# Optimization experiments

Hardware: AMD Instinct MI355X
Metric: run time of the kernel (lower is better)

The kernel has to match this reference:

```python
import jax, jax.numpy as jnp
import numpy as np

D_MODEL = 1024
NUM_HEADS = 16
THETA = 10000.0


def _rope(x, pos):
    # x: [B, H, S, d_k], pos: [B, S] int
    d = x.shape[-1]
    half = d // 2
    inv_freq = THETA ** (-(jnp.arange(half, dtype=jnp.float32) * 2.0) / d)  # [half]
    ang = pos.astype(jnp.float32)[..., None] * inv_freq                     # [B, S, half]
    cos = jnp.cos(ang)[:, None, :, :]  # [B, 1, S, half]
    sin = jnp.sin(ang)[:, None, :, :]
    x1 = x[..., 0::2]
    x2 = x[..., 1::2]
    r1 = x1 * cos - x2 * sin
    r2 = x1 * sin + x2 * cos
    return jnp.stack([r1, r2], axis=-1).reshape(x.shape)


def setup_inputs() -> dict:
    key = jax.random.key(0)
    ks = jax.random.split(key, 5)
    B, S, D = 2, 2048, D_MODEL
    scale = 1.0 / np.sqrt(D)
    x = jax.random.normal(ks[0], (B, S, D), dtype=jnp.float32)
    token_positions = jnp.broadcast_to(jnp.arange(S, dtype=jnp.int32), (B, S))
    Wq = jax.random.normal(ks[1], (D, D), dtype=jnp.float32) * scale
    Wk = jax.random.normal(ks[2], (D, D), dtype=jnp.float32) * scale
    Wv = jax.random.normal(ks[3], (D, D), dtype=jnp.float32) * scale
    Wo = jax.random.normal(ks[4], (D, D), dtype=jnp.float32) * scale
    return {"x": x, "token_positions": token_positions, "Wq": Wq, "Wk": Wk, "Wv": Wv, "Wo": Wo}


def reference(x, token_positions, Wq, Wk, Wv, Wo):
    B, S, D = x.shape
    H = NUM_HEADS
    dk = D // H
    # Linear: y = x @ W.T (torch nn.Linear convention, no bias)
    q = jnp.einsum('bsd,od->bso', x, Wq).reshape(B, S, H, dk).transpose(0, 2, 1, 3)
    k = jnp.einsum('bsd,od->bso', x, Wk).reshape(B, S, H, dk).transpose(0, 2, 1, 3)
    v = jnp.einsum('bsd,od->bso', x, Wv).reshape(B, S, H, dk).transpose(0, 2, 1, 3)
    q = _rope(q, token_positions)
    k = _rope(k, token_positions)
    scores = jnp.einsum('bhqd,bhkd->bhqk', q, k) / jnp.sqrt(jnp.float32(dk))
    causal = jnp.tril(jnp.ones((S, S), dtype=bool))
    scores = jnp.where(causal, scores, jnp.finfo(scores.dtype).min)
    attn = jax.nn.softmax(scores, axis=-1)
    out = jnp.einsum('bhqk,bhkd->bhqd', attn, v)  # [B, H, S, dk]
    out = out.transpose(0, 2, 1, 3).reshape(B, S, D)
    return jnp.einsum('bsd,od->bso', out, Wo)
```

## Files before the change

kernel.cpp:

```cpp
#include <hip/hip_runtime.h>
#include <stdint.h>

#define S_LEN 2048
#define DMODEL 1024
#define NHEAD 16
#define DK 64
#define BATCH 2

typedef __attribute__((ext_vector_type(8))) short bf16x8;
typedef __attribute__((ext_vector_type(4))) float f32x4;

__device__ __forceinline__ unsigned short f2bf(float f) {
  union { float f; unsigned u; } x; x.f = f;
  unsigned u = x.u;
  return (unsigned short)((u + 0x7fffu + ((u >> 16) & 1u)) >> 16);
}

__device__ __forceinline__ uint cvt_pk_bf16(float a, float b) {
  uint r;
  asm("v_cvt_pk_bf16_f32 %0, %1, %2" : "=v"(r) : "v"(a), "v"(b));
  return r;
}

__device__ __forceinline__ void gload_lds16(const void* g, void* l) {
  __builtin_amdgcn_global_load_lds(
      (const __attribute__((address_space(1))) unsigned int*)g,
      (__attribute__((address_space(3))) unsigned int*)l, 16, 0, 0);
}

#define QSCALE 0.18033688011112042f

__global__ __launch_bounds__(256) void cast_inputs(
    const float4* __restrict__ x,
    const float4* __restrict__ wq, const float4* __restrict__ wk,
    const float4* __restrict__ wv, const float4* __restrict__ wo,
    ushort4* __restrict__ xb, ushort4* __restrict__ wqkvb, ushort4* __restrict__ wob,
    const int* __restrict__ pos, float2* __restrict__ rope)
{
  int i = blockIdx.x * 256 + threadIdx.x;
  const int NCAST = (1 << 21);
  if (i < NCAST) {
    float4 v; ushort4* dst;
    if (i < (1 << 20)) {
      v = x[i]; dst = xb + i;
    } else {
      int j = i - (1 << 20);
      int wsel = j >> 18;
      int o = j & ((1 << 18) - 1);
      const float4* src = (wsel == 0) ? wq : (wsel == 1) ? wk : (wsel == 2) ? wv : wo;
      v = src[o];
      dst = (wsel < 3) ? (wqkvb + ((size_t)wsel << 18) + o) : (wob + o);
    }
    ushort4 r;
    r.x = f2bf(v.x); r.y = f2bf(v.y); r.z = f2bf(v.z); r.w = f2bf(v.w);
    *dst = r;
  } else {
    int idx = i - NCAST;
    if (idx < 4096 * 32) {
      int ps = idx >> 5;
      int fi = idx & 31;
      float p = (float)pos[ps];
      float freq = exp2f(-(float)fi * 0.41524101186092096f);
      float ang = p * freq;
      rope[idx] = make_float2(cosf(ang), sinf(ang));
    }
  }
}

__global__ __launch_bounds__(256) void gemm_qkv(
    const ushort* __restrict__ A, const ushort* __restrict__ Bw,
    const float2* __restrict__ rope,
    ushort* __restrict__ Qb, ushort* __restrict__ Kb, ushort* __restrict__ Vg)
{
  constexpr int Kdim = 1024;
  __shared__ ushort At[128 * 64];
  __shared__ ushort Bt[128 * 64];
  const int bm = blockIdx.x & 31;
  const int bn = blockIdx.x >> 5;
  const int tid = threadIdx.x;
  const int w = tid >> 6, lane = tid & 63;
  const int wr = w >> 1, wc = w & 1;
  const int lrow = lane >> 3;
  const int lch = lane & 7;

  f32x4 acc[4][4];
#pragma unroll
  for (int i = 0; i < 4; ++i)
#pragma unroll
    for (int j = 0; j < 4; ++j) acc[i][j] = (f32x4){0.f, 0.f, 0.f, 0.f};

  const size_t abase = (size_t)(bm * 128) * Kdim;
  const size_t bbase = (size_t)(bn * 128) * Kdim;

  for (int kt = 0; kt < Kdim / 64; ++kt) {
#pragma unroll
    for (int inst = 0; inst < 4; ++inst) {
      int r = w * 32 + inst * 8 + lrow;
      int gc = lch ^ (r & 7);
      gload_lds16(A + abase + (size_t)r * Kdim + kt * 64 + gc * 8,
                  &At[(w * 32 + inst * 8) * 64]);
      gload_lds16(Bw + bbase + (size_t)r * Kdim + kt * 64 + gc * 8,
                  &Bt[(w * 32 + inst * 8) * 64]);
    }
    __syncthreads();
    __builtin_amdgcn_s_setprio(1);
#pragma unroll
    for (int kk = 0; kk < 2; ++kk) {
      bf16x8 af[4], bfv[4];
      int ch = kk * 4 + (lane >> 4);
#pragma unroll
      for (int fm = 0; fm < 4; ++fm) {
        int row = wr * 64 + fm * 16 + (lane & 15);
        af[fm] = *(const bf16x8*)&At[row * 64 + ((ch ^ (row & 7)) << 3)];
      }
#pragma unroll
      for (int fn = 0; fn < 4; ++fn) {
        int row = wc * 64 + fn * 16 + (lane & 15);
        bfv[fn] = *(const bf16x8*)&Bt[row * 64 + ((ch ^ (row & 7)) << 3)];
      }
#pragma unroll
      for (int fm = 0; fm < 4; ++fm)
#pragma unroll
        for (int fn = 0; fn < 4; ++fn)
          acc[fm][fn] = __builtin_amdgcn_mfma_f32_16x16x32_bf16(
              af[fm], bfv[fn], acc[fm][fn], 0, 0, 0);
    }
    __builtin_amdgcn_s_setprio(0);
    __syncthreads();
  }

  const int sel = bn >> 3;
  if (sel == 2) {
#pragma unroll
    for (int fn = 0; fn < 4; ++fn) {
      int gn = bn * 128 + wc * 64 + fn * 16 + (lane & 15);
      int col = gn & 1023;
      int h = col >> 6, d = col & 63;
#pragma unroll
      for (int fm = 0; fm < 4; ++fm) {
        int gm0 = bm * 128 + wr * 64 + fm * 16 + ((lane >> 4) << 2);
        int b = gm0 >> 11, s0 = gm0 & 2047;
        uint lo = cvt_pk_bf16(acc[fm][fn][0], acc[fm][fn][1]);
        uint hi2 = cvt_pk_bf16(acc[fm][fn][2], acc[fm][fn][3]);
        uint2 val; val.x = lo; val.y = hi2;
        *(uint2*)(Vg + ((size_t)((b * NHEAD + h) * DK + d) * S_LEN) + s0) = val;
      }
    }
  } else {
    ushort* dst0 = (sel == 0) ? Qb : Kb;
#pragma unroll
    for (int fn = 0; fn < 4; ++fn) {
      int gn = bn * 128 + wc * 64 + fn * 16 + (lane & 15);
      int col = gn & 1023;
      int h = col >> 6, d = col & 63;
#pragma unroll
      for (int fm = 0; fm < 4; ++fm) {
        int gm0 = bm * 128 + wr * 64 + fm * 16 + ((lane >> 4) << 2);
#pragma unroll
        for (int j = 0; j < 4; ++j) {
          int gm = gm0 + j;
          float v = acc[fm][fn][j];
          float p = __shfl_xor(v, 1);
          float2 cs = rope[gm * 32 + (d >> 1)];
          float r = (d & 1) ? (v * cs.x + p * cs.y) : (v * cs.x - p * cs.y);
          if (sel == 0) r *= QSCALE;
          int b = gm >> 11, s = gm & 2047;
          dst0[((size_t)(b * NHEAD + h) * S_LEN + s) * DK + d] = f2bf(r);
        }
      }
    }
  }
}

__global__ __launch_bounds__(256) void gemm_out64(
    const ushort* __restrict__ A, const ushort* __restrict__ Bw,
    float* __restrict__ Out)
{
  constexpr int Kdim = 1024;
  __shared__ ushort At[64 * 64];
  __shared__ ushort Bt[128 * 64];
  const int bm = blockIdx.x & 63;
  const int bn = blockIdx.x >> 6;
  const int tid = threadIdx.x;
  const int w = tid >> 6, lane = tid & 63;
  const int wr = w >> 1, wc = w & 1;
  const int lrow = lane >> 3;
  const int lch = lane & 7;

  f32x4 acc[2][4];
#pragma unroll
  for (int i = 0; i < 2; ++i)
#pragma unroll
    for (int j = 0; j < 4; ++j) acc[i][j] = (f32x4){0.f, 0.f, 0.f, 0.f};

  const size_t abase = (size_t)(bm * 64) * Kdim;
  const size_t bbase = (size_t)(bn * 128) * Kdim;

  for (int kt = 0; kt < Kdim / 64; ++kt) {
#pragma unroll
    for (int inst = 0; inst < 2; ++inst) {
      int r = inst * 32 + w * 8 + lrow;
      int gc = lch ^ (r & 7);
      gload_lds16(A + abase + (size_t)r * Kdim + kt * 64 + gc * 8,
                  &At[(inst * 32 + w * 8) * 64]);
    }
#pragma unroll
    for (int inst = 0; inst < 4; ++inst) {
      int r = inst * 32 + w * 8 + lrow;
      int gc = lch ^ (r & 7);
      gload_lds16(Bw + bbase + (size_t)r * Kdim + kt * 64 + gc * 8,
                  &Bt[(inst * 32 + w * 8) * 64]);
    }
    __syncthreads();
    __builtin_amdgcn_s_setprio(1);
#pragma unroll
    for (int kk = 0; kk < 2; ++kk) {
      bf16x8 af[2], bfv[4];
      int ch = kk * 4 + (lane >> 4);
#pragma unroll
      for (int fm = 0; fm < 2; ++fm) {
        int row = wr * 32 + fm * 16 + (lane & 15);
        af[fm] = *(const bf16x8*)&At[row * 64 + ((ch ^ (row & 7)) << 3)];
      }
#pragma unroll
      for (int fn = 0; fn < 4; ++fn) {
        int row = wc * 64 + fn * 16 + (lane & 15);
        bfv[fn] = *(const bf16x8*)&Bt[row * 64 + ((ch ^ (row & 7)) << 3)];
      }
#pragma unroll
      for (int fm = 0; fm < 2; ++fm)
#pragma unroll
        for (int fn = 0; fn < 4; ++fn)
          acc[fm][fn] = __builtin_amdgcn_mfma_f32_16x16x32_bf16(
              af[fm], bfv[fn], acc[fm][fn], 0, 0, 0);
    }
    __builtin_amdgcn_s_setprio(0);
    __syncthreads();
  }

#pragma unroll
  for (int fn = 0; fn < 4; ++fn) {
    int gn = bn * 128 + wc * 64 + fn * 16 + (lane & 15);
#pragma unroll
    for (int fm = 0; fm < 2; ++fm) {
      int gm0 = bm * 64 + wr * 32 + fm * 16 + ((lane >> 4) << 2);
#pragma unroll
      for (int j = 0; j < 4; ++j)
        Out[(size_t)(gm0 + j) * 1024 + gn] = acc[fm][fn][j];
    }
  }
}

__global__ __launch_bounds__(256) void attn_kernel(
    const ushort* __restrict__ Qb, const ushort* __restrict__ Kb,
    const ushort* __restrict__ Vg, ushort* __restrict__ Ob)
{
  __shared__ ushort Kt[2][64 * 64];
  __shared__ ushort Vt[2][64 * 64];
  __shared__ ushort Pt[4][16 * 64];
  const int tid = threadIdx.x;
  const int w = tid >> 6, lane = tid & 63;
  const int g = lane >> 4, q = lane & 15;
  const int ww = w & 1;
  const int bid = blockIdx.x;
  const int swz = (bid & 7) * 128 + (bid >> 3);
  const int bh = swz >> 5;
  const int pair = (swz >> 1) & 15;
  const int half = swz & 1;
  const size_t kqbase = (size_t)bh * (S_LEN * DK);
  const size_t vbase  = (size_t)bh * (DK * S_LEN);
  const int b = bh >> 4, h = bh & 15;
  const int qtw = (w < 2) ? (31 - pair) : pair;
  const int ktmax = 31 - pair;
  const int qrow0 = qtw * 64 + half * 32 + ww * 16;
  ushort* Pw = Pt[w];
  uint* Pw32 = (uint*)Pw;

  bf16x8 qf[2];
  {
    const ushort* qp = Qb + kqbase + (size_t)(qrow0 + q) * DK + g * 8;
    qf[0] = *(const bf16x8*)qp;
    qf[1] = *(const bf16x8*)(qp + 32);
  }
  f32x4 oacc[4];
#pragma unroll
  for (int dt = 0; dt < 4; ++dt) oacc[dt] = (f32x4){0.f, 0.f, 0.f, 0.f};
  float m_r = -INFINITY, l_r = 0.f;

#define STAGE(buf_, kt_)                                                     \
  do {                                                                       \
    _Pragma("unroll") for (int pass = 0; pass < 2; ++pass) {                 \
      int r0 = pass * 32 + w * 8;                                            \
      int r = r0 + (lane >> 3);                                              \
      int gc = (lane & 7) ^ (r & 7);                                         \
      gload_lds16(Kb + kqbase + (size_t)((kt_) * 64 + r) * DK + gc * 8,      \
                  &Kt[buf_][r0 * 64]);                                       \
      gload_lds16(Vg + vbase + (size_t)r * S_LEN + (kt_) * 64 + gc * 8,      \
                  &Vt[buf_][r0 * 64]);                                       \
    }                                                                        \
  } while (0)

  STAGE(0, 0);
  __syncthreads();

  int cur = 0;
  for (int kt = 0; kt <= ktmax; ++kt) {
    if (kt < ktmax) STAGE(cur ^ 1, kt + 1);

    if (kt <= qtw) {
      f32x4 sacc[4];
#pragma unroll
      for (int ct = 0; ct < 4; ++ct) sacc[ct] = (f32x4){0.f, 0.f, 0.f, 0.f};
      __builtin_amdgcn_s_setprio(1);
#pragma unroll
      for (int kk = 0; kk < 2; ++kk) {
        int ch = kk * 4 + g;
#pragma unroll
        for (int ct = 0; ct < 4; ++ct) {
          int row = ct * 16 + q;
          bf16x8 kf = *(const bf16x8*)&Kt[cur][row * 64 + ((ch ^ (row & 7)) << 3)];
          sacc[ct] = __builtin_amdgcn_mfma_f32_16x16x32_bf16(kf, qf[kk], sacc[ct], 0, 0, 0);
        }
      }
      __builtin_amdgcn_s_setprio(0);

      if (kt == qtw) {
        int qa = qrow0 + q;
#pragma unroll
        for (int ct = 0; ct < 4; ++ct) {
#pragma unroll
          for (int j = 0; j < 4; ++j) {
            int kv = qtw * 64 + ct * 16 + g * 4 + j;
            if (kv > qa) sacc[ct][j] = -INFINITY;
          }
        }
      }

      float mx = sacc[0][0];
#pragma unroll
      for (int ct = 0; ct < 4; ++ct)
#pragma unroll
        for (int j = 0; j < 4; ++j) mx = fmaxf(mx, sacc[ct][j]);
      mx = fmaxf(mx, __shfl_xor(mx, 16));
      mx = fmaxf(mx, __shfl_xor(mx, 32));
      if (mx > m_r + 8.0f) {
        float sc = exp2f(m_r - mx);
        m_r = mx;
        l_r *= sc;
#pragma unroll
        for (int dt = 0; dt < 4; ++dt)
#pragma unroll
          for (int j = 0; j < 4; ++j) oacc[dt][j] *= sc;
      }
      float p[4][4];
      float rs = 0.f;
#pragma unroll
      for (int ct = 0; ct < 4; ++ct)
#pragma unroll
        for (int j = 0; j < 4; ++j) {
          float e = exp2f(sacc[ct][j] - m_r);
          p[ct][j] = e; rs += e;
        }
      rs += __shfl_xor(rs, 16);
      rs += __shfl_xor(rs, 32);
      l_r += rs;

#pragma unroll
      for (int ct = 0; ct < 4; ++ct)
#pragma unroll
        for (int i = 0; i < 2; ++i) {
          uint u = cvt_pk_bf16(p[ct][2 * i], p[ct][2 * i + 1]);
          int idx = 8 * ct + 2 * g + i;
          Pw32[q * 32 + (((idx >> 2) ^ (q & 7)) << 2) + (idx & 3)] = u;
        }
      __builtin_amdgcn_s_setprio(1);
#pragma unroll
      for (int kk = 0; kk < 2; ++kk) {
        int ch = kk * 4 + g;
        bf16x8 pb = *(const bf16x8*)&Pw[q * 64 + ((ch ^ (q & 7)) << 3)];
#pragma unroll
        for (int dt = 0; dt < 4; ++dt) {
          int vr = dt * 16 + q;
          bf16x8 vf = *(const bf16x8*)&Vt[cur][vr * 64 + ((ch ^ (vr & 7)) << 3)];
          oacc[dt] = __builtin_amdgcn_mfma_f32_16x16x32_bf16(vf, pb, oacc[dt], 0, 0, 0);
        }
      }
      __builtin_amdgcn_s_setprio(0);
    }

    __syncthreads();
    cur ^= 1;
  }

  float inv = 1.0f / l_r;
#pragma unroll
  for (int dt = 0; dt < 4; ++dt)
#pragma unroll
    for (int i = 0; i < 2; ++i) {
      uint u = cvt_pk_bf16(oacc[dt][2 * i] * inv, oacc[dt][2 * i + 1] * inv);
      int idx = dt * 8 + 2 * g + i;
      Pw32[q * 32 + (((idx >> 2) ^ (q & 7)) << 2) + (idx & 3)] = u;
    }
#pragma unroll
  for (int pass = 0; pass < 2; ++pass) {
    int qr = pass * 8 + (lane >> 3), c = lane & 7;
    bf16x8 vv = *(const bf16x8*)&Pw[qr * 64 + ((c ^ (qr & 7)) << 3)];
    *(bf16x8*)(Ob + ((size_t)(b * S_LEN) + qrow0 + qr) * DMODEL + h * DK + c * 8) = vv;
  }
#undef STAGE
}

extern "C" void kernel_launch(void* const* d_in, const int* in_sizes, int n_in,
                              void* d_out, int out_size, void* d_ws, size_t ws_size,
                              hipStream_t stream) {
  const float* x  = (const float*)d_in[0];
  const int* pos  = (const int*)d_in[1];
  const float* wq = (const float*)d_in[2];
  const float* wk = (const float*)d_in[3];
  const float* wv = (const float*)d_in[4];
  const float* wo = (const float*)d_in[5];
  float* out = (float*)d_out;

  char* ws = (char*)d_ws;
  ushort* xb    = (ushort*)(ws);
  ushort* wqkvb = (ushort*)(ws + (size_t)( 8u << 20));
  ushort* wob   = (ushort*)(ws + (size_t)(14u << 20));
  float2* rope  = (float2*)(ws + (size_t)(16u << 20));
  ushort* Qb    = (ushort*)(ws + (size_t)(17u << 20));
  ushort* Kb    = (ushort*)(ws + (size_t)(25u << 20));
  ushort* Vg    = (ushort*)(ws + (size_t)(33u << 20));
  ushort* Ob    = (ushort*)(ws + (size_t)(41u << 20));

  cast_inputs<<<8704, 256, 0, stream>>>((const float4*)x, (const float4*)wq,
      (const float4*)wk, (const float4*)wv, (const float4*)wo,
      (ushort4*)xb, (ushort4*)wqkvb, (ushort4*)wob, pos, rope);
  gemm_qkv<<<32 * 24, 256, 0, stream>>>(xb, wqkvb, rope, Qb, Kb, Vg);
  attn_kernel<<<1024, 256, 0, stream>>>(Qb, Kb, Vg, Ob);
  gemm_out64<<<512, 256, 0, stream>>>(Ob, wob, out);
}
```

Measured before the change: 127.3 us.

## Process paired query tiles sequentially per block with full 64-row tiles

Each attention block now handles two complementary query tiles (pair and 31-pair) one after the other, with all four waves covering 64 query rows, instead of splitting waves across two tiles in a shared KV loop. This halves the grid and lets every staged K/V tile be used by all four waves, removing the idle waves that skipped causal tiles. The row-sum cross-lane shuffle is also moved out of the inner loop to a single reduction at the end. The cost is fewer blocks and two serialized KV sweeps per block.

```diff
diff --git a/kernel.cpp b/kernel.cpp
--- a/kernel.cpp
+++ b/kernel.cpp
@@ -261,53 +261,56 @@
   const int tid = threadIdx.x;
   const int w = tid >> 6, lane = tid & 63;
   const int g = lane >> 4, q = lane & 15;
-  const int ww = w & 1;
   const int bid = blockIdx.x;
-  const int swz = (bid & 7) * 128 + (bid >> 3);
-  const int bh = swz >> 5;
-  const int pair = (swz >> 1) & 15;
-  const int half = swz & 1;
+  const int swz = (bid & 7) * 64 + (bid >> 3);
+  const int bh = swz >> 4, pair = swz & 15;
   const size_t kqbase = (size_t)bh * (S_LEN * DK);
   const size_t vbase  = (size_t)bh * (DK * S_LEN);
   const int b = bh >> 4, h = bh & 15;
-  const int qtw = (w < 2) ? (31 - pair) : pair;
-  const int ktmax = 31 - pair;
-  const int qrow0 = qtw * 64 + half * 32 + ww * 16;
   ushort* Pw = Pt[w];
   uint* Pw32 = (uint*)Pw;
 
-  bf16x8 qf[2];
-  {
-    const ushort* qp = Qb + kqbase + (size_t)(qrow0 + q) * DK + g * 8;
-    qf[0] = *(const bf16x8*)qp;
-    qf[1] = *(const bf16x8*)(qp + 32);
-  }
-  f32x4 oacc[4];
-#pragma unroll
-  for (int dt = 0; dt < 4; ++dt) oacc[dt] = (f32x4){0.f, 0.f, 0.f, 0.f};
-  float m_r = -INFINITY, l_r = 0.f;
-
-#define STAGE(buf_, kt_)                                                     \
-  do {                                                                       \
-    _Pragma("unroll") for (int pass = 0; pass < 2; ++pass) {                 \
-      int r0 = pass * 32 + w * 8;                                            \
-      int r = r0 + (lane >> 3);                                              \
-      int gc = (lane & 7) ^ (r & 7);                                         \
-      gload_lds16(Kb + kqbase + (size_t)((kt_) * 64 + r) * DK + gc * 8,      \
-                  &Kt[buf_][r0 * 64]);                                       \
-      gload_lds16(Vg + vbase + (size_t)r * S_LEN + (kt_) * 64 + gc * 8,      \
-                  &Vt[buf_][r0 * 64]);                                       \
-    }                                                                        \
-  } while (0)
-
-  STAGE(0, 0);
-  __syncthreads();
-
-  int cur = 0;
-  for (int kt = 0; kt <= ktmax; ++kt) {
-    if (kt < ktmax) STAGE(cur ^ 1, kt + 1);
-
-    if (kt <= qtw) {
+  for (int t2 = 0; t2 < 2; ++t2) {
+    const int qt = t2 ? (31 - pair) : pair;
+    const int qrow0 = qt * 64 + w * 16;
+
+    bf16x8 qf[2];
+    {
+      const ushort* qp = Qb + kqbase + (size_t)(qrow0 + q) * DK + g * 8;
+      qf[0] = *(const bf16x8*)qp;
+      qf[1] = *(const bf16x8*)(qp + 32);
+    }
+    f32x4 oacc[4];
+#pragma unroll
+    for (int dt = 0; dt < 4; ++dt) oacc[dt] = (f32x4){0.f, 0.f, 0.f, 0.f};
+    float m_r = -INFINITY, l_r = 0.f;
+
+#pragma unroll
+    for (int pass = 0; pass < 2; ++pass) {
+      int r0 = pass * 32 + w * 8;
+      int r = r0 + (lane >> 3);
+      int gc = (lane & 7) ^ (r & 7);
+      gload_lds16(Kb + kqbase + (size_t)r * DK + gc * 8, &Kt[0][r0 * 64]);
+      gload_lds16(Vg + vbase + (size_t)r * S_LEN + gc * 8, &Vt[0][r0 * 64]);
+    }
+    __syncthreads();
+
+    int cur = 0;
+    for (int kt = 0; kt <= qt; ++kt) {
+      if (kt < qt) {
+        int nxt = cur ^ 1, ktn = kt + 1;
+#pragma unroll
+        for (int pass = 0; pass < 2; ++pass) {
+          int r0 = pass * 32 + w * 8;
+          int r = r0 + (lane >> 3);
+          int gc = (lane & 7) ^ (r & 7);
+          gload_lds16(Kb + kqbase + (size_t)(ktn * 64 + r) * DK + gc * 8,
+                      &Kt[nxt][r0 * 64]);
+          gload_lds16(Vg + vbase + (size_t)r * S_LEN + ktn * 64 + gc * 8,
+                      &Vt[nxt][r0 * 64]);
+        }
+      }
+
       f32x4 sacc[4];
 #pragma unroll
       for (int ct = 0; ct < 4; ++ct) sacc[ct] = (f32x4){0.f, 0.f, 0.f, 0.f};
@@ -324,13 +327,13 @@
       }
       __builtin_amdgcn_s_setprio(0);
 
-      if (kt == qtw) {
+      if (kt == qt) {
         int qa = qrow0 + q;
 #pragma unroll
         for (int ct = 0; ct < 4; ++ct) {
 #pragma unroll
           for (int j = 0; j < 4; ++j) {
-            int kv = qtw * 64 + ct * 16 + g * 4 + j;
+            int kv = qt * 64 + ct * 16 + g * 4 + j;
             if (kv > qa) sacc[ct][j] = -INFINITY;
           }
         }
@@ -361,8 +364,6 @@
           float e = exp2f(sacc[ct][j] - m_r);
           p[ct][j] = e; rs += e;
         }
-      rs += __shfl_xor(rs, 16);
-      rs += __shfl_xor(rs, 32);
       l_r += rs;
 
 #pragma unroll
@@ -386,28 +387,29 @@
         }
       }
       __builtin_amdgcn_s_setprio(0);
-    }
-
-    __syncthreads();
-    cur ^= 1;
-  }
-
-  float inv = 1.0f / l_r;
-#pragma unroll
-  for (int dt = 0; dt < 4; ++dt)
-#pragma unroll
-    for (int i = 0; i < 2; ++i) {
-      uint u = cvt_pk_bf16(oacc[dt][2 * i] * inv, oacc[dt][2 * i + 1] * inv);
-      int idx = dt * 8 + 2 * g + i;
-      Pw32[q * 32 + (((idx >> 2) ^ (q & 7)) << 2) + (idx & 3)] = u;
-    }
-#pragma unroll
-  for (int pass = 0; pass < 2; ++pass) {
-    int qr = pass * 8 + (lane >> 3), c = lane & 7;
-    bf16x8 vv = *(const bf16x8*)&Pw[qr * 64 + ((c ^ (qr & 7)) << 3)];
-    *(bf16x8*)(Ob + ((size_t)(b * S_LEN) + qrow0 + qr) * DMODEL + h * DK + c * 8) = vv;
-  }
-#undef STAGE
+      __syncthreads();
+      cur ^= 1;
+    }
+
+    float lt = l_r;
+    lt += __shfl_xor(lt, 16);
+    lt += __shfl_xor(lt, 32);
+    float inv = 1.0f / lt;
+#pragma unroll
+    for (int dt = 0; dt < 4; ++dt)
+#pragma unroll
+      for (int i = 0; i < 2; ++i) {
+        uint u = cvt_pk_bf16(oacc[dt][2 * i] * inv, oacc[dt][2 * i + 1] * inv);
+        int idx = dt * 8 + 2 * g + i;
+        Pw32[q * 32 + (((idx >> 2) ^ (q & 7)) << 2) + (idx & 3)] = u;
+      }
+#pragma unroll
+    for (int pass = 0; pass < 2; ++pass) {
+      int qr = pass * 8 + (lane >> 3), c = lane & 7;
+      bf16x8 vv = *(const bf16x8*)&Pw[qr * 64 + ((c ^ (qr & 7)) << 3)];
+      *(bf16x8*)(Ob + ((size_t)(b * S_LEN) + qrow0 + qr) * DMODEL + h * DK + c * 8) = vv;
+    }
+  }
 }
 
 extern "C" void kernel_launch(void* const* d_in, const int* in_sizes, int n_in,
@@ -435,6 +437,6 @@
       (const float4*)wk, (const float4*)wv, (const float4*)wo,
       (ushort4*)xb, (ushort4*)wqkvb, (ushort4*)wob, pos, rope);
   gemm_qkv<<<32 * 24, 256, 0, stream>>>(xb, wqkvb, rope, Qb, Kb, Vg);
-  attn_kernel<<<1024, 256, 0, stream>>>(Qb, Kb, Vg, Ob);
+  attn_kernel<<<512, 256, 0, stream>>>(Qb, Kb, Vg, Ob);
   gemm_out64<<<512, 256, 0, stream>>>(Ob, wob, out);
 }
```

Measured after the change: 119.5 us, median of 3. 1.07x faster.

## Process paired causal query tiles per block sharing each staged K/V tile

Applied to the files above, without the earlier changes.

Each attention block now handles two full 64-row query tiles (tile 31-pair and tile pair) with all four waves working on both, instead of splitting the pair across waves and halves. Each K/V tile staged into LDS is reused by both query tiles, and the grid shrinks from 1024 to 512 blocks. The per-tile row-sum shuffle reduction is deferred to the epilogue, removing two cross-lane shuffles per tile step. In exchange each thread holds double the accumulators, which raises register pressure, and fewer blocks are available to fill the CUs.

```diff
diff --git a/kernel.cpp b/kernel.cpp
--- a/kernel.cpp
+++ b/kernel.cpp
@@ -261,31 +261,38 @@
   const int tid = threadIdx.x;
   const int w = tid >> 6, lane = tid & 63;
   const int g = lane >> 4, q = lane & 15;
-  const int ww = w & 1;
   const int bid = blockIdx.x;
-  const int swz = (bid & 7) * 128 + (bid >> 3);
-  const int bh = swz >> 5;
-  const int pair = (swz >> 1) & 15;
-  const int half = swz & 1;
+  const int swz = (bid & 7) * 64 + (bid >> 3);
+  const int bh = swz >> 4, pair = swz & 15;
   const size_t kqbase = (size_t)bh * (S_LEN * DK);
   const size_t vbase  = (size_t)bh * (DK * S_LEN);
   const int b = bh >> 4, h = bh & 15;
-  const int qtw = (w < 2) ? (31 - pair) : pair;
-  const int ktmax = 31 - pair;
-  const int qrow0 = qtw * 64 + half * 32 + ww * 16;
   ushort* Pw = Pt[w];
   uint* Pw32 = (uint*)Pw;
 
-  bf16x8 qf[2];
+  const int qtA = 31 - pair;
+  const int qtB = pair;
+  const int ktmax = qtA;
+  const int qrow0A = qtA * 64 + w * 16;
+  const int qrow0B = qtB * 64 + w * 16;
+
+  bf16x8 qfA[2], qfB[2];
   {
-    const ushort* qp = Qb + kqbase + (size_t)(qrow0 + q) * DK + g * 8;
-    qf[0] = *(const bf16x8*)qp;
-    qf[1] = *(const bf16x8*)(qp + 32);
-  }
-  f32x4 oacc[4];
-#pragma unroll
-  for (int dt = 0; dt < 4; ++dt) oacc[dt] = (f32x4){0.f, 0.f, 0.f, 0.f};
-  float m_r = -INFINITY, l_r = 0.f;
+    const ushort* qpA = Qb + kqbase + (size_t)(qrow0A + q) * DK + g * 8;
+    qfA[0] = *(const bf16x8*)qpA;
+    qfA[1] = *(const bf16x8*)(qpA + 32);
+    const ushort* qpB = Qb + kqbase + (size_t)(qrow0B + q) * DK + g * 8;
+    qfB[0] = *(const bf16x8*)qpB;
+    qfB[1] = *(const bf16x8*)(qpB + 32);
+  }
+  f32x4 oaccA[4], oaccB[4];
+#pragma unroll
+  for (int dt = 0; dt < 4; ++dt) {
+    oaccA[dt] = (f32x4){0.f, 0.f, 0.f, 0.f};
+    oaccB[dt] = (f32x4){0.f, 0.f, 0.f, 0.f};
+  }
+  float mA = -INFINITY, lA = 0.f;
+  float mB = -INFINITY, lB = 0.f;
 
 #define STAGE(buf_, kt_)                                                     \
   do {                                                                       \
@@ -300,6 +307,94 @@
     }                                                                        \
   } while (0)
 
+#define TILE_STEP(qt_, qrow0_, qf_, oacc_, m_, l_)                           \
+  do {                                                                       \
+    f32x4 sacc[4];                                                           \
+    _Pragma("unroll") for (int ct = 0; ct < 4; ++ct)                         \
+      sacc[ct] = (f32x4){0.f, 0.f, 0.f, 0.f};                                \
+    __builtin_amdgcn_s_setprio(1);                                           \
+    _Pragma("unroll") for (int kk = 0; kk < 2; ++kk) {                       \
+      int ch = kk * 4 + g;                                                   \
+      _Pragma("unroll") for (int ct = 0; ct < 4; ++ct) {                     \
+        int row = ct * 16 + q;                                               \
+        bf16x8 kf = *(const bf16x8*)                                         \
+            &Kt[cur][row * 64 + ((ch ^ (row & 7)) << 3)];                    \
+        sacc[ct] = __builtin_amdgcn_mfma_f32_16x16x32_bf16(                  \
+            kf, qf_[kk], sacc[ct], 0, 0, 0);                                 \
+      }                                                                      \
+    }                                                                        \
+    __builtin_amdgcn_s_setprio(0);                                           \
+    if (kt == (qt_)) {                     \
+      int qa = (qrow0_) + q;                                                 \
+      _Pragma("unroll") for (int ct = 0; ct < 4; ++ct)                       \
+        _Pragma("unroll") for (int j = 0; j < 4; ++j) {                      \
+          int kv = (qt_) * 64 + ct * 16 + g * 4 + j;                         \
+          if (kv > qa) sacc[ct][j] = -INFINITY;                              \
+        }                                                                    \
+    }                                                                        \
+    float mx = sacc[0][0];                                                   \
+    _Pragma("unroll") for (int ct = 0; ct < 4; ++ct)                         \
+      _Pragma("unroll") for (int j = 0; j < 4; ++j)                          \
+        mx = fmaxf(mx, sacc[ct][j]);                                         \
+    mx = fmaxf(mx, __shfl_xor(mx, 16));                                      \
+    mx = fmaxf(mx, __shfl_xor(mx, 32));                                      \
+    if (mx > (m_) + 8.0f) {                      \
+      float sc = exp2f((m_) - mx);                                           \
+      (m_) = mx;                                                             \
+      (l_) *= sc;                                                            \
+      _Pragma("unroll") for (int dt = 0; dt < 4; ++dt)                       \
+        _Pragma("unroll") for (int j = 0; j < 4; ++j) oacc_[dt][j] *= sc;    \
+    }                                                                        \
+    float p[4][4];                                                           \
+    float rs = 0.f;                                                          \
+    _Pragma("unroll") for (int ct = 0; ct < 4; ++ct)                         \
+      _Pragma("unroll") for (int j = 0; j < 4; ++j) {                        \
+        float e = exp2f(sacc[ct][j] - (m_));                                 \
+        p[ct][j] = e; rs += e;                                               \
+      }                                                                      \
+    (l_) += rs;                           \
+    _Pragma("unroll") for (int ct = 0; ct < 4; ++ct)                         \
+      _Pragma("unroll") for (int i = 0; i < 2; ++i) {                        \
+        uint u = cvt_pk_bf16(p[ct][2 * i], p[ct][2 * i + 1]);                \
+        int idx = 8 * ct + 2 * g + i;                            \
+        Pw32[q * 32 + (((idx >> 2) ^ (q & 7)) << 2) + (idx & 3)] = u;        \
+      }                                                                      \
+    __builtin_amdgcn_s_setprio(1);                                           \
+    _Pragma("unroll") for (int kk = 0; kk < 2; ++kk) {                       \
+      int ch = kk * 4 + g;                                                   \
+      bf16x8 pb = *(const bf16x8*)&Pw[q * 64 + ((ch ^ (q & 7)) << 3)];       \
+      _Pragma("unroll") for (int dt = 0; dt < 4; ++dt) {                     \
+        int vr = dt * 16 + q;                                                \
+        bf16x8 vf = *(const bf16x8*)                                         \
+            &Vt[cur][vr * 64 + ((ch ^ (vr & 7)) << 3)];                      \
+        oacc_[dt] = __builtin_amdgcn_mfma_f32_16x16x32_bf16(                 \
+            vf, pb, oacc_[dt], 0, 0, 0);                                     \
+      }                                                                      \
+    }                                                                        \
+    __builtin_amdgcn_s_setprio(0);                                           \
+  } while (0)
+
+#define EPILOGUE(qrow0_, oacc_, l_)                                          \
+  do {                                                                       \
+    float lt = (l_);                                                         \
+    lt += __shfl_xor(lt, 16);                                                \
+    lt += __shfl_xor(lt, 32);                                                \
+    float inv = 1.0f / lt;                                                   \
+    _Pragma("unroll") for (int dt = 0; dt < 4; ++dt)                         \
+      _Pragma("unroll") for (int i = 0; i < 2; ++i) {                        \
+        uint u = cvt_pk_bf16(oacc_[dt][2 * i] * inv,                         \
+                             oacc_[dt][2 * i + 1] * inv);                    \
+        int idx = dt * 8 + 2 * g + i;                             \
+        Pw32[q * 32 + (((idx >> 2) ^ (q & 7)) << 2) + (idx & 3)] = u;        \
+      }                                                                      \
+    _Pragma("unroll") for (int pass = 0; pass < 2; ++pass) {                 \
+      int qr = pass * 8 + (lane >> 3), c = lane & 7;                         \
+      bf16x8 vv = *(const bf16x8*)&Pw[qr * 64 + ((c ^ (qr & 7)) << 3)];      \
+      *(bf16x8*)(Ob + ((size_t)(b * S_LEN) + (qrow0_) + qr) * DMODEL +       \
+                 h * DK + c * 8) = vv;                                       \
+    }                                                                        \
+  } while (0)
+
   STAGE(0, 0);
   __syncthreads();
 
@@ -307,107 +402,18 @@
   for (int kt = 0; kt <= ktmax; ++kt) {
     if (kt < ktmax) STAGE(cur ^ 1, kt + 1);
 
-    if (kt <= qtw) {
-      f32x4 sacc[4];
-#pragma unroll
-      for (int ct = 0; ct < 4; ++ct) sacc[ct] = (f32x4){0.f, 0.f, 0.f, 0.f};
-      __builtin_amdgcn_s_setprio(1);
-#pragma unroll
-      for (int kk = 0; kk < 2; ++kk) {
-        int ch = kk * 4 + g;
-#pragma unroll
-        for (int ct = 0; ct < 4; ++ct) {
-          int row = ct * 16 + q;
-          bf16x8 kf = *(const bf16x8*)&Kt[cur][row * 64 + ((ch ^ (row & 7)) << 3)];
-          sacc[ct] = __builtin_amdgcn_mfma_f32_16x16x32_bf16(kf, qf[kk], sacc[ct], 0, 0, 0);
-        }
-      }
-      __builtin_amdgcn_s_setprio(0);
-
-      if (kt == qtw) {
-        int qa = qrow0 + q;
-#pragma unroll
-        for (int ct = 0; ct < 4; ++ct) {
-#pragma unroll
-          for (int j = 0; j < 4; ++j) {
-            int kv = qtw * 64 + ct * 16 + g * 4 + j;
-            if (kv > qa) sacc[ct][j] = -INFINITY;
-          }
-        }
-      }
-
-      float mx = sacc[0][0];
-#pragma unroll
-      for (int ct = 0; ct < 4; ++ct)
-#pragma unroll
-        for (int j = 0; j < 4; ++j) mx = fmaxf(mx, sacc[ct][j]);
-      mx = fmaxf(mx, __shfl_xor(mx, 16));
-      mx = fmaxf(mx, __shfl_xor(mx, 32));
-      if (mx > m_r + 8.0f) {
-        float sc = exp2f(m_r - mx);
-        m_r = mx;
-        l_r *= sc;
-#pragma unroll
-        for (int dt = 0; dt < 4; ++dt)
-#pragma unroll
-          for (int j = 0; j < 4; ++j) oacc[dt][j] *= sc;
-      }
-      float p[4][4];
-      float rs = 0.f;
-#pragma unroll
-      for (int ct = 0; ct < 4; ++ct)
-#pragma unroll
-        for (int j = 0; j < 4; ++j) {
-          float e = exp2f(sacc[ct][j] - m_r);
-          p[ct][j] = e; rs += e;
-        }
-      rs += __shfl_xor(rs, 16);
-      rs += __shfl_xor(rs, 32);
-      l_r += rs;
-
-#pragma unroll
-      for (int ct = 0; ct < 4; ++ct)
-#pragma unroll
-        for (int i = 0; i < 2; ++i) {
-          uint u = cvt_pk_bf16(p[ct][2 * i], p[ct][2 * i + 1]);
-          int idx = 8 * ct + 2 * g + i;
-          Pw32[q * 32 + (((idx >> 2) ^ (q & 7)) << 2) + (idx & 3)] = u;
-        }
-      __builtin_amdgcn_s_setprio(1);
-#pragma unroll
-      for (int kk = 0; kk < 2; ++kk) {
-        int ch = kk * 4 + g;
-        bf16x8 pb = *(const bf16x8*)&Pw[q * 64 + ((ch ^ (q & 7)) << 3)];
-#pragma unroll
-        for (int dt = 0; dt < 4; ++dt) {
-          int vr = dt * 16 + q;
-          bf16x8 vf = *(const bf16x8*)&Vt[cur][vr * 64 + ((ch ^ (vr & 7)) << 3)];
-          oacc[dt] = __builtin_amdgcn_mfma_f32_16x16x32_bf16(vf, pb, oacc[dt], 0, 0, 0);
-        }
-      }
-      __builtin_amdgcn_s_setprio(0);
-    }
+    TILE_STEP(qtA, qrow0A, qfA, oaccA, mA, lA);
+    if (kt <= qtB) TILE_STEP(qtB, qrow0B, qfB, oaccB, mB, lB);
 
     __syncthreads();
     cur ^= 1;
   }
 
-  float inv = 1.0f / l_r;
-#pragma unroll
-  for (int dt = 0; dt < 4; ++dt)
-#pragma unroll
-    for (int i = 0; i < 2; ++i) {
-      uint u = cvt_pk_bf16(oacc[dt][2 * i] * inv, oacc[dt][2 * i + 1] * inv);
-      int idx = dt * 8 + 2 * g + i;
-      Pw32[q * 32 + (((idx >> 2) ^ (q & 7)) << 2) + (idx & 3)] = u;
-    }
-#pragma unroll
-  for (int pass = 0; pass < 2; ++pass) {
-    int qr = pass * 8 + (lane >> 3), c = lane & 7;
-    bf16x8 vv = *(const bf16x8*)&Pw[qr * 64 + ((c ^ (qr & 7)) << 3)];
-    *(bf16x8*)(Ob + ((size_t)(b * S_LEN) + qrow0 + qr) * DMODEL + h * DK + c * 8) = vv;
-  }
+  EPILOGUE(qrow0A, oaccA, lA);
+  EPILOGUE(qrow0B, oaccB, lB);
 #undef STAGE
+#undef TILE_STEP
+#undef EPILOGUE
 }
 
 extern "C" void kernel_launch(void* const* d_in, const int* in_sizes, int n_in,
@@ -435,6 +441,6 @@
       (const float4*)wk, (const float4*)wv, (const float4*)wo,
       (ushort4*)xb, (ushort4*)wqkvb, (ushort4*)wob, pos, rope);
   gemm_qkv<<<32 * 24, 256, 0, stream>>>(xb, wqkvb, rope, Qb, Kb, Vg);
-  attn_kernel<<<1024, 256, 0, stream>>>(Qb, Kb, Vg, Ob);
+  attn_kernel<<<512, 256, 0, stream>>>(Qb, Kb, Vg, Ob);
   gemm_out64<<<512, 256, 0, stream>>>(Ob, wob, out);
 }
```

New measurement: 120.3 us. 1.06x faster.
